# Kernel tuning notes

Hardware: AMD Instinct MI355X
Metric: run time of the kernel (lower is better)

## Reference

```python
import jax, jax.numpy as jnp
import numpy as np

SIZE = 256

def _linear(x, W, b):
    # torch nn.Linear: y = x @ W^T + b, W has shape [out, in]
    return jnp.einsum('bsd,ed->bse', x, W) + b

def setup_inputs() -> dict:
    key = jax.random.key(0)
    ks = jax.random.split(key, 10)
    B, Sq, Sk, D = 8, 2048, 2048, SIZE
    s = 1.0 / np.sqrt(D)
    return {
        'x': jax.random.normal(ks[0], (B, Sq, D), jnp.float32),
        'states': jax.random.normal(ks[1], (B, Sk, D), jnp.float32),
        'Wq': jax.random.normal(ks[2], (D, D), jnp.float32) * s,
        'bq': jnp.zeros((D,), jnp.float32),
        'Wk': jax.random.normal(ks[3], (D, D), jnp.float32) * s,
        'bk': jnp.zeros((D,), jnp.float32),
        'Wv': jax.random.normal(ks[4], (D, D), jnp.float32) * s,
        'bv': jnp.zeros((D,), jnp.float32),
        'Wa': jax.random.normal(ks[5], (D, D), jnp.float32) * s,  # LuongAttention.fc
        'ba': jnp.zeros((D,), jnp.float32),
    }

def reference(x, states, Wq, bq, Wk, bk, Wv, bv, Wa, ba):
    q = _linear(x, Wq, bq)          # [B,Sq,D]
    k = _linear(states, Wk, bk)     # [B,Sk,D]
    v = _linear(states, Wv, bv)     # [B,Sk,D]
    wk = _linear(k, Wa, ba)         # [B,Sk,D]
    scores = jnp.einsum('bqd,bkd->bqk', q, wk)   # bmm(q, wk^T)
    scores = jax.nn.softmax(scores, axis=-1)
    # original: (v[:,None,:,:] * scores[...,None]).sum(-2) == matmul
    context = jnp.einsum('bqk,bkd->bqd', scores, v)
    return context
```

## Files before the change

kernel.cpp:

```cpp
#include <hip/hip_runtime.h>
#include <cstdint>
#include <cstddef>

typedef _Float16 half_t;
typedef _Float16 half8 __attribute__((ext_vector_type(8)));
typedef _Float16 half4v __attribute__((ext_vector_type(4)));
typedef float float4_ __attribute__((ext_vector_type(4)));

#define NB 8
#define SEQ 2048
#define DIM 256
#define NROWS (NB*SEQ)
#define KS 4
#define NIT 16

__device__ __forceinline__ void dma16(const half_t* g, half_t* l) {
    __builtin_amdgcn_global_load_lds(
        (const __attribute__((address_space(1))) void*)g,
        (__attribute__((address_space(3))) void*)l,
        16, 0, 0);
}

__global__ __launch_bounds__(256) void prep_kernel(
    const float* __restrict__ Wq, const float* __restrict__ Wk,
    const float* __restrict__ Wv, const float* __restrict__ Wa,
    const float* __restrict__ bq,
    half_t* __restrict__ M_hi, half_t* __restrict__ M_lo,
    half_t* __restrict__ Wk_hi, half_t* __restrict__ Wk_lo,
    half_t* __restrict__ Wv_hi, float* __restrict__ bq2)
{
    const int d = blockIdx.x;
    const int m = threadIdx.x;
    const int idx = d * 256 + m;
    float acc = 0.f;
    for (int e = 0; e < 256; ++e)
        acc += Wa[e * 256 + d] * Wq[e * 256 + m];
    half_t h = (half_t)acc;
    M_hi[idx] = h;
    M_lo[idx] = (half_t)(acc - (float)h);
    float wk = Wk[idx];
    h = (half_t)wk;
    Wk_hi[idx] = h;
    Wk_lo[idx] = (half_t)(wk - (float)h);
    Wv_hi[idx] = (half_t)Wv[idx];
    if (m == 0) {
        float b2 = 0.f;
        for (int e = 0; e < 256; ++e) b2 += bq[e] * Wa[e * 256 + d];
        bq2[d] = b2;
    }
}

__global__ __launch_bounds__(256, 2) void linear_kernel(
    const float* __restrict__ x, const float* __restrict__ states,
    const half_t* __restrict__ M_hi, const half_t* __restrict__ M_lo, const float* __restrict__ bq2,
    const half_t* __restrict__ Wk_hi, const half_t* __restrict__ Wk_lo, const float* __restrict__ bk,
    const half_t* __restrict__ Wv_hi, const float* __restrict__ bv,
    half_t* __restrict__ q2_hi,
    half_t* __restrict__ k_hi,
    half_t* __restrict__ vT)
{
    __shared__ half_t sB[2 * 64 * 256];
    half_t* sBh = sB;
    half_t* sBl = sB + 64 * 256;

    const int seg  = blockIdx.x >> 8;
    const int t    = blockIdx.x & 255;
    const int tid  = threadIdx.x;
    const int lane = tid & 63;
    const int wv   = tid >> 6;
    const int quad = lane >> 4;
    const int l15  = lane & 15;
    const int rb   = t * 64;
    const int r0   = rb + wv * 16;

    const float* src  = (seg == 0) ? x : states;
    const half_t* Bh  = (seg == 0) ? M_hi : (seg == 1) ? Wk_hi : Wv_hi;
    const half_t* Bl  = (seg == 0) ? M_lo : Wk_lo;
    const float* bias = (seg == 0) ? bq2 : (seg == 1) ? bk : bv;

    half8 ah[8], al[8];
    #pragma unroll
    for (int c = 0; c < 8; ++c) {
        const float* pa = src + (size_t)(r0 + l15) * 256 + c * 32 + quad * 8;
        float4_ u0 = *(const float4_*)pa;
        float4_ u1 = *(const float4_*)(pa + 4);
        #pragma unroll
        for (int j = 0; j < 4; ++j) {
            half_t hh = (half_t)u0[j];
            ah[c][j] = hh; al[c][j] = (half_t)(u0[j] - (float)hh);
            hh = (half_t)u1[j];
            ah[c][4 + j] = hh; al[c][4 + j] = (half_t)(u1[j] - (float)hh);
        }
    }

    float4_ acc[16];
    if (seg != 2) {
        #pragma unroll
        for (int nt = 0; nt < 16; ++nt) {
            float be = bias[nt * 16 + l15];
            acc[nt] = {be, be, be, be};
        }
    } else {
        #pragma unroll
        for (int et = 0; et < 16; ++et)
            #pragma unroll
            for (int r = 0; r < 4; ++r)
                acc[et][r] = bias[et * 16 + quad * 4 + r];
    }

    #pragma unroll
    for (int eg = 0; eg < 4; ++eg) {
        __syncthreads();
        #pragma unroll
        for (int i = 0; i < 8; ++i) {
            int g = tid + i * 256;
            int e = g >> 5, c = g & 31;
            *(half8*)(sBh + e * 256 + ((c ^ (e & 7)) * 8)) =
                *(const half8*)(Bh + (size_t)(eg * 64 + e) * 256 + c * 8);
        }
        if (seg != 2) {
            #pragma unroll
            for (int i = 0; i < 8; ++i) {
                int g = tid + i * 256;
                int e = g >> 5, c = g & 31;
                *(half8*)(sBl + e * 256 + ((c ^ (e & 7)) * 8)) =
                    *(const half8*)(Bl + (size_t)(eg * 64 + e) * 256 + c * 8);
            }
        }
        __syncthreads();

        if (seg != 2) {
            #pragma unroll
            for (int ntl = 0; ntl < 4; ++ntl) {
                float4_ a = acc[eg * 4 + ntl];
                const int el = ntl * 16 + l15;
                #pragma unroll
                for (int c = 0; c < 8; ++c) {
                    int off = el * 256 + (((c * 4 + quad) ^ (el & 7)) * 8);
                    half8 bh = *(const half8*)(sBh + off);
                    half8 bl = *(const half8*)(sBl + off);
                    a = __builtin_amdgcn_mfma_f32_16x16x32_f16(ah[c], bh, a, 0, 0, 0);
                    a = __builtin_amdgcn_mfma_f32_16x16x32_f16(al[c], bh, a, 0, 0, 0);
                    a = __builtin_amdgcn_mfma_f32_16x16x32_f16(ah[c], bl, a, 0, 0, 0);
                }
                acc[eg * 4 + ntl] = a;
            }
        } else {
            #pragma unroll
            for (int ntl = 0; ntl < 4; ++ntl) {
                float4_ a = acc[eg * 4 + ntl];
                const int el = ntl * 16 + l15;
                #pragma unroll
                for (int c = 0; c < 8; ++c) {
                    int off = el * 256 + (((c * 4 + quad) ^ (el & 7)) * 8);
                    half8 aw = *(const half8*)(sBh + off);
                    a = __builtin_amdgcn_mfma_f32_16x16x32_f16(aw, ah[c], a, 0, 0, 0);
                }
                acc[eg * 4 + ntl] = a;
            }
        }
    }

    __syncthreads();
    if (seg != 2) {
        half_t* R = sB;
        #pragma unroll
        for (int nt = 0; nt < 16; ++nt)
            #pragma unroll
            for (int r = 0; r < 4; ++r)
                R[(wv * 16 + quad * 4 + r) * 256 + nt * 16 + l15] = (half_t)acc[nt][r];
        __syncthreads();
        if (seg == 0) {
            for (int i = 0; i < 8; ++i) {
                int g = tid + i * 256;
                int row = g >> 5, cc = g & 31;
                *(half8*)(q2_hi + (size_t)(rb + row) * 256 + cc * 8) =
                    *(const half8*)(R + row * 256 + cc * 8);
            }
        } else {
            for (int i = 0; i < 8; ++i) {
                int g = tid + i * 256;
                int row = g >> 5, cc = g & 31;
                int s = row & 31;
                size_t dst = ((size_t)(rb + row) >> 5) * 8192 + s * 256 + ((cc ^ (s & 7)) * 8);
                *(half8*)(k_hi + dst) = *(const half8*)(R + row * 256 + cc * 8);
            }
        }
    } else {
        half_t* sV = sB;
        #pragma unroll
        for (int et = 0; et < 16; ++et)
            #pragma unroll
            for (int r = 0; r < 4; ++r)
                sV[(et * 16 + quad * 4 + r) * 68 + wv * 16 + l15] = (half_t)acc[et][r];
        __syncthreads();
        const int b = rb >> 11, s0 = rb & 2047;
        for (int i = 0; i < 8; ++i) {
            int g = tid + i * 256;
            int d = g >> 3, sc8 = g & 7;
            int kt = (s0 >> 5) + (sc8 >> 2);
            int q  = sc8 & 3;
            int t32 = (sc8 >> 2) * 32;
            int slot = q ^ (d & 3) ^ ((d >> 2) & 3);
            half4v a4 = *(const half4v*)(sV + d * 68 + t32 + q * 4);
            half4v b4 = *(const half4v*)(sV + d * 68 + t32 + 16 + q * 4);
            half8 hv;
            hv[0] = a4[0]; hv[1] = a4[1]; hv[2] = a4[2]; hv[3] = a4[3];
            hv[4] = b4[0]; hv[5] = b4[1]; hv[6] = b4[2]; hv[7] = b4[3];
            size_t dst = ((size_t)b * 64 + kt) * 8192 + d * 32 + slot * 8;
            *(half8*)(vT + dst) = hv;
        }
    }
}

__global__ __launch_bounds__(256, 2) void attn_kernel(
    const half_t* __restrict__ q2_hi,
    const half_t* __restrict__ k_hi, const half_t* __restrict__ vT,
    half_t* __restrict__ pc, float* __restrict__ pm, float* __restrict__ pl)
{
    __shared__ __align__(16) unsigned char smem[64 * 1024];
    float* scr = (float*)smem;

    const int tid  = threadIdx.x;
    const int lane = tid & 63;
    const int wv   = tid >> 6;
    const int quad = lane >> 4;
    const int l15  = lane & 15;

    const int b  = blockIdx.x & 7;
    const int qt = (blockIdx.x >> 3) & 15;
    const int ks = blockIdx.x >> 7;

    const int qbase = b * 2048 + qt * 128 + wv * 32;

    half8 qf[2][8];
    #pragma unroll
    for (int ct = 0; ct < 2; ++ct)
        #pragma unroll
        for (int c = 0; c < 8; ++c)
            qf[ct][c] = *(const half8*)(q2_hi +
                (size_t)(qbase + ct * 16 + l15) * 256 + c * 32 + quad * 8);

    float4_ ctx[16][2];
    #pragma unroll
    for (int dt = 0; dt < 16; ++dt) {
        ctx[dt][0] = {0.f, 0.f, 0.f, 0.f};
        ctx[dt][1] = {0.f, 0.f, 0.f, 0.f};
    }
    float m_c[2] = {-1e30f, -1e30f};
    float l_c[2] = {0.f, 0.f};

    const half_t* kh_b = k_hi + (size_t)b * 64 * 8192;
    const half_t* vt_b = vT   + (size_t)b * 64 * 8192;
    const int t0 = ks * NIT;

    const int vslot8 = (quad ^ (l15 & 3) ^ ((l15 >> 2) & 3)) * 8;

    {
        const half_t* kt_ = kh_b + (size_t)t0 * 8192;
        #pragma unroll
        for (int i = 0; i < 4; ++i) {
            const int sg = i * 4 + wv;
            dma16(kt_ + sg * 512 + lane * 8, (half_t*)smem + sg * 512);
        }
        const half_t* vt_ = vt_b + (size_t)t0 * 8192;
        #pragma unroll
        for (int i = 0; i < 4; ++i) {
            const int sg = i * 4 + wv;
            dma16(vt_ + sg * 512 + lane * 8, (half_t*)(smem + 32768) + sg * 512);
        }
    }

    half8 pfp[2];
    #pragma unroll
    for (int ct = 0; ct < 2; ++ct)
        #pragma unroll
        for (int j = 0; j < 8; ++j) pfp[ct][j] = (half_t)0;

    for (int it = 0; it < NIT; ++it) {
        half_t* s_k  = (half_t*)(smem + ((it & 1) << 14));
        half_t* s_vP = (half_t*)(smem + 32768 + (((it + 1) & 1) << 14));
        const bool pre = (it + 1 < NIT);

        asm volatile("s_waitcnt vmcnt(4)" ::: "memory");
        __builtin_amdgcn_s_barrier();
        asm volatile("" ::: "memory");

        if (pre) {
            const half_t* kt_ = kh_b + (size_t)(t0 + it + 1) * 8192;
            half_t* kdst = (half_t*)(smem + (((it + 1) & 1) << 14));
            #pragma unroll
            for (int i = 0; i < 4; ++i) {
                const int sg = i * 4 + wv;
                dma16(kt_ + sg * 512 + lane * 8, kdst + sg * 512);
            }
        }

        float4_ S[2][2];
        S[0][0] = {0.f,0.f,0.f,0.f}; S[0][1] = {0.f,0.f,0.f,0.f};
        S[1][0] = {0.f,0.f,0.f,0.f}; S[1][1] = {0.f,0.f,0.f,0.f};
        __builtin_amdgcn_s_setprio(1);
        #pragma unroll
        for (int c = 0; c < 8; ++c)
            #pragma unroll
            for (int kt = 0; kt < 2; ++kt) {
                const int key = kt * 16 + l15;
                const int off = key * 256 + (((c * 4 + quad) ^ (key & 7)) * 8);
                half8 kf = *(const half8*)(s_k + off);
                #pragma unroll
                for (int ct = 0; ct < 2; ++ct)
                    S[kt][ct] = __builtin_amdgcn_mfma_f32_16x16x32_f16(kf, qf[ct][c], S[kt][ct], 0, 0, 0);
            }
        __builtin_amdgcn_s_setprio(0);

        float mx0, mx1;
        {
            float a0 = fmaxf(fmaxf(S[0][0][0], S[0][0][1]), fmaxf(S[0][0][2], S[0][0][3]));
            float b0 = fmaxf(fmaxf(S[1][0][0], S[1][0][1]), fmaxf(S[1][0][2], S[1][0][3]));
            mx0 = fmaxf(a0, b0);
            mx0 = fmaxf(mx0, __shfl_xor(mx0, 16));
            mx0 = fmaxf(mx0, __shfl_xor(mx0, 32));
            float a1 = fmaxf(fmaxf(S[0][1][0], S[0][1][1]), fmaxf(S[0][1][2], S[0][1][3]));
            float b1 = fmaxf(fmaxf(S[1][1][0], S[1][1][1]), fmaxf(S[1][1][2], S[1][1][3]));
            mx1 = fmaxf(a1, b1);
            mx1 = fmaxf(mx1, __shfl_xor(mx1, 16));
            mx1 = fmaxf(mx1, __shfl_xor(mx1, 32));
        }
        const int doresc = __any((mx0 > m_c[0] + 8.f) || (mx1 > m_c[1] + 8.f));
        float alpha0 = 1.f, alpha1 = 1.f;
        if (doresc) {
            float mn0 = fmaxf(m_c[0], mx0);
            float mn1 = fmaxf(m_c[1], mx1);
            alpha0 = __expf(m_c[0] - mn0);
            alpha1 = __expf(m_c[1] - mn1);
            m_c[0] = mn0; m_c[1] = mn1;
        }

        __builtin_amdgcn_s_setprio(1);
        if (it > 0) {
            #pragma unroll
            for (int dt = 0; dt < 16; ++dt) {
                half8 vf = *(const half8*)(s_vP + (dt * 16 + l15) * 32 + vslot8);
                ctx[dt][0] = __builtin_amdgcn_mfma_f32_16x16x32_f16(vf, pfp[0], ctx[dt][0], 0, 0, 0);
                ctx[dt][1] = __builtin_amdgcn_mfma_f32_16x16x32_f16(vf, pfp[1], ctx[dt][1], 0, 0, 0);
            }
        }

        half8 pfc[2];
        #pragma unroll
        for (int ct = 0; ct < 2; ++ct) {
            const float mm = m_c[ct];
            float rs = 0.f;
            #pragma unroll
            for (int r = 0; r < 4; ++r) {
                float p0 = __expf(S[0][ct][r] - mm);
                float p1 = __expf(S[1][ct][r] - mm);
                rs += p0 + p1;
                pfc[ct][r]     = (half_t)p0;
                pfc[ct][4 + r] = (half_t)p1;
            }
            rs += __shfl_xor(rs, 16);
            rs += __shfl_xor(rs, 32);
            l_c[ct] = l_c[ct] * (ct ? alpha1 : alpha0) + rs;
        }
        __builtin_amdgcn_s_setprio(0);

        if (doresc) {
            #pragma unroll
            for (int dt = 0; dt < 16; ++dt)
                #pragma unroll
                for (int r = 0; r < 4; ++r) {
                    ctx[dt][0][r] *= alpha0;
                    ctx[dt][1][r] *= alpha1;
                }
        }

        pfp[0] = pfc[0];
        pfp[1] = pfc[1];

        if (pre) {
            __builtin_amdgcn_sched_barrier(0);
            __builtin_amdgcn_s_barrier();
            asm volatile("" ::: "memory");
            const half_t* vt_ = vt_b + (size_t)(t0 + it + 1) * 8192;
            half_t* vdst = (half_t*)(smem + 32768 + (((it + 1) & 1) << 14));
            #pragma unroll
            for (int i = 0; i < 4; ++i) {
                const int sg = i * 4 + wv;
                dma16(vt_ + sg * 512 + lane * 8, vdst + sg * 512);
            }
        }
    }

    asm volatile("s_waitcnt vmcnt(0)" ::: "memory");
    __builtin_amdgcn_s_barrier();
    asm volatile("" ::: "memory");
    {
        half_t* s_v = (half_t*)(smem + 32768 + (((NIT - 1) & 1) << 14));
        __builtin_amdgcn_s_setprio(1);
        #pragma unroll
        for (int dt = 0; dt < 16; ++dt) {
            half8 vf = *(const half8*)(s_v + (dt * 16 + l15) * 32 + vslot8);
            ctx[dt][0] = __builtin_amdgcn_mfma_f32_16x16x32_f16(vf, pfp[0], ctx[dt][0], 0, 0, 0);
            ctx[dt][1] = __builtin_amdgcn_mfma_f32_16x16x32_f16(vf, pfp[1], ctx[dt][1], 0, 0, 0);
        }
        __builtin_amdgcn_s_setprio(0);
    }

    float rinv[2] = {1.0f / l_c[0], 1.0f / l_c[1]};
    float* sw = scr + wv * (32 * 68);
    half_t* pcs = pc + (size_t)ks * NROWS * 256;
    #pragma unroll
    for (int rd = 0; rd < 4; ++rd) {
        #pragma unroll
        for (int dtl = 0; dtl < 4; ++dtl) {
            const int dt = rd * 4 + dtl;
            #pragma unroll
            for (int ct = 0; ct < 2; ++ct)
                #pragma unroll
                for (int r = 0; r < 4; ++r)
                    sw[(ct * 16 + l15) * 68 + dtl * 16 + quad * 4 + r] = ctx[dt][ct][r] * rinv[ct];
        }
        #pragma unroll
        for (int i = 0; i < 8; ++i) {
            int g = lane + i * 64;
            int q = g >> 4, dc = g & 15;
            float4_ v4 = *(const float4_*)(sw + q * 68 + dc * 4);
            half4v h4;
            #pragma unroll
            for (int j = 0; j < 4; ++j) h4[j] = (half_t)v4[j];
            *(half4v*)(pcs + (size_t)(qbase + q) * 256 + rd * 64 + dc * 4) = h4;
        }
    }
    if (quad == 0) {
        #pragma unroll
        for (int ct = 0; ct < 2; ++ct) {
            const size_t row = qbase + ct * 16 + l15;
            pm[(size_t)ks * NROWS + row] = m_c[ct];
            pl[(size_t)ks * NROWS + row] = l_c[ct];
        }
    }
}

__global__ __launch_bounds__(256) void combine_kernel(
    const half_t* __restrict__ pc, const float* __restrict__ pm,
    const float* __restrict__ pl, float* __restrict__ out)
{
    const int t = threadIdx.x;
    const int row = blockIdx.x * 4 + (t >> 6);
    const int d0 = (t & 63) * 4;
    float m[KS], l[KS];
    float ms = -1e30f;
    #pragma unroll
    for (int i = 0; i < KS; ++i) {
        m[i] = pm[(size_t)i * NROWS + row];
        l[i] = pl[(size_t)i * NROWS + row];
        ms = fmaxf(ms, m[i]);
    }
    float w[KS], tot = 0.f;
    #pragma unroll
    for (int i = 0; i < KS; ++i) {
        w[i] = l[i] * __expf(m[i] - ms);
        tot += w[i];
    }
    float inv = 1.0f / tot;
    float4_ o = {0.f, 0.f, 0.f, 0.f};
    #pragma unroll
    for (int i = 0; i < KS; ++i) {
        half4v y = *(const half4v*)(pc + ((size_t)i * NROWS + row) * 256 + d0);
        float wi = w[i] * inv;
        #pragma unroll
        for (int j = 0; j < 4; ++j) o[j] += wi * (float)y[j];
    }
    *(float4_*)(out + (size_t)row * 256 + d0) = o;
}

extern "C" void kernel_launch(void* const* d_in, const int* in_sizes, int n_in,
                              void* d_out, int out_size, void* d_ws, size_t ws_size,
                              hipStream_t stream) {
    const float* x      = (const float*)d_in[0];
    const float* states = (const float*)d_in[1];
    const float* Wq     = (const float*)d_in[2];
    const float* bq     = (const float*)d_in[3];
    const float* Wk     = (const float*)d_in[4];
    const float* bk     = (const float*)d_in[5];
    const float* Wv     = (const float*)d_in[6];
    const float* bv     = (const float*)d_in[7];
    const float* Wa     = (const float*)d_in[8];
    float* out = (float*)d_out;

    char* ws = (char*)d_ws;
    size_t off = 0;
    auto alloc = [&](size_t bytes) -> void* {
        void* p = ws + off;
        off += (bytes + 255) & ~(size_t)255;
        return p;
    };
    half_t* M_hi  = (half_t*)alloc(65536 * 2);
    half_t* M_lo  = (half_t*)alloc(65536 * 2);
    half_t* Wk_hi = (half_t*)alloc(65536 * 2);
    half_t* Wk_lo = (half_t*)alloc(65536 * 2);
    half_t* Wv_hi = (half_t*)alloc(65536 * 2);
    float*  bq2   = (float*)alloc(256 * 4);
    half_t* q2_hi = (half_t*)alloc((size_t)NROWS * 256 * 2);
    half_t* k_hi  = (half_t*)alloc((size_t)NROWS * 256 * 2);
    half_t* vT    = (half_t*)alloc((size_t)NROWS * 256 * 2);
    half_t* pc    = (half_t*)alloc((size_t)KS * NROWS * 256 * 2);
    float*  pm    = (float*)alloc((size_t)KS * NROWS * 4);
    float*  pl    = (float*)alloc((size_t)KS * NROWS * 4);

    prep_kernel<<<256, 256, 0, stream>>>(Wq, Wk, Wv, Wa, bq,
                                         M_hi, M_lo, Wk_hi, Wk_lo, Wv_hi, bq2);
    linear_kernel<<<768, 256, 0, stream>>>(x, states,
                                           M_hi, M_lo, bq2,
                                           Wk_hi, Wk_lo, bk,
                                           Wv_hi, bv,
                                           q2_hi, k_hi, vT);
    attn_kernel<<<8 * 16 * KS, 256, 0, stream>>>(q2_hi, k_hi, vT,
                                                 pc, pm, pl);
    combine_kernel<<<NROWS / 4, 256, 0, stream>>>(pc, pm, pl, out);
}
```

Before: 196.8 us.

## Interleave PV MFMAs with QK MFMAs and defer cross-lane softmax reductions

Moves the previous tile's P·V MFMAs into the QK score loop so the two matrix streams interleave, and issues the V prefetch earlier, right after the score loop. Per-lane row sums are now kept unreduced and shuffled only once at the end. The max reduction across lanes now runs only when a rescale is triggered. This removes shuffle latency from the inner loop and gives the scheduler more independent MFMA work, at the cost of higher register pressure and a changed barrier placement. Lanes can now see different partial maxima before reduction, and correctness rests on the lazy-rescale threshold.

```diff
diff --git a/kernel.cpp b/kernel.cpp
--- a/kernel.cpp
+++ b/kernel.cpp
@@ -301,7 +301,7 @@
         S[1][0] = {0.f,0.f,0.f,0.f}; S[1][1] = {0.f,0.f,0.f,0.f};
         __builtin_amdgcn_s_setprio(1);
         #pragma unroll
-        for (int c = 0; c < 8; ++c)
+        for (int c = 0; c < 8; ++c) {
             #pragma unroll
             for (int kt = 0; kt < 2; ++kt) {
                 const int key = kt * 16 + l15;
@@ -311,41 +311,53 @@
                 for (int ct = 0; ct < 2; ++ct)
                     S[kt][ct] = __builtin_amdgcn_mfma_f32_16x16x32_f16(kf, qf[ct][c], S[kt][ct], 0, 0, 0);
             }
+            if (it > 0) {
+                #pragma unroll
+                for (int dl = 0; dl < 2; ++dl) {
+                    const int dt = c * 2 + dl;
+                    half8 vf = *(const half8*)(s_vP + (dt * 16 + l15) * 32 + vslot8);
+                    ctx[dt][0] = __builtin_amdgcn_mfma_f32_16x16x32_f16(vf, pfp[0], ctx[dt][0], 0, 0, 0);
+                    ctx[dt][1] = __builtin_amdgcn_mfma_f32_16x16x32_f16(vf, pfp[1], ctx[dt][1], 0, 0, 0);
+                }
+            }
+        }
         __builtin_amdgcn_s_setprio(0);
+        __builtin_amdgcn_sched_barrier(0);
+        __builtin_amdgcn_s_barrier();
+        asm volatile("" ::: "memory");
+
+        if (pre) {
+            const half_t* vt_ = vt_b + (size_t)(t0 + it + 1) * 8192;
+            half_t* vdst = (half_t*)(smem + 32768 + (((it + 1) & 1) << 14));
+            #pragma unroll
+            for (int i = 0; i < 4; ++i) {
+                const int sg = i * 4 + wv;
+                dma16(vt_ + sg * 512 + lane * 8, vdst + sg * 512);
+            }
+        }
 
         float mx0, mx1;
         {
             float a0 = fmaxf(fmaxf(S[0][0][0], S[0][0][1]), fmaxf(S[0][0][2], S[0][0][3]));
             float b0 = fmaxf(fmaxf(S[1][0][0], S[1][0][1]), fmaxf(S[1][0][2], S[1][0][3]));
             mx0 = fmaxf(a0, b0);
-            mx0 = fmaxf(mx0, __shfl_xor(mx0, 16));
-            mx0 = fmaxf(mx0, __shfl_xor(mx0, 32));
             float a1 = fmaxf(fmaxf(S[0][1][0], S[0][1][1]), fmaxf(S[0][1][2], S[0][1][3]));
             float b1 = fmaxf(fmaxf(S[1][1][0], S[1][1][1]), fmaxf(S[1][1][2], S[1][1][3]));
             mx1 = fmaxf(a1, b1);
-            mx1 = fmaxf(mx1, __shfl_xor(mx1, 16));
-            mx1 = fmaxf(mx1, __shfl_xor(mx1, 32));
         }
         const int doresc = __any((mx0 > m_c[0] + 8.f) || (mx1 > m_c[1] + 8.f));
         float alpha0 = 1.f, alpha1 = 1.f;
         if (doresc) {
-            float mn0 = fmaxf(m_c[0], mx0);
-            float mn1 = fmaxf(m_c[1], mx1);
+            float r0 = fmaxf(mx0, __shfl_xor(mx0, 16));
+            r0 = fmaxf(r0, __shfl_xor(r0, 32));
+            float r1 = fmaxf(mx1, __shfl_xor(mx1, 16));
+            r1 = fmaxf(r1, __shfl_xor(r1, 32));
+            float mn0 = fmaxf(m_c[0], r0);
+            float mn1 = fmaxf(m_c[1], r1);
             alpha0 = __expf(m_c[0] - mn0);
             alpha1 = __expf(m_c[1] - mn1);
             m_c[0] = mn0; m_c[1] = mn1;
         }
-
-        __builtin_amdgcn_s_setprio(1);
-        if (it > 0) {
-            #pragma unroll
-            for (int dt = 0; dt < 16; ++dt) {
-                half8 vf = *(const half8*)(s_vP + (dt * 16 + l15) * 32 + vslot8);
-                ctx[dt][0] = __builtin_amdgcn_mfma_f32_16x16x32_f16(vf, pfp[0], ctx[dt][0], 0, 0, 0);
-                ctx[dt][1] = __builtin_amdgcn_mfma_f32_16x16x32_f16(vf, pfp[1], ctx[dt][1], 0, 0, 0);
-            }
-        }
-
         half8 pfc[2];
         #pragma unroll
         for (int ct = 0; ct < 2; ++ct) {
@@ -359,12 +371,8 @@
                 pfc[ct][r]     = (half_t)p0;
                 pfc[ct][4 + r] = (half_t)p1;
             }
-            rs += __shfl_xor(rs, 16);
-            rs += __shfl_xor(rs, 32);
             l_c[ct] = l_c[ct] * (ct ? alpha1 : alpha0) + rs;
         }
-        __builtin_amdgcn_s_setprio(0);
-
         if (doresc) {
             #pragma unroll
             for (int dt = 0; dt < 16; ++dt)
@@ -374,22 +382,8 @@
                     ctx[dt][1][r] *= alpha1;
                 }
         }
-
         pfp[0] = pfc[0];
         pfp[1] = pfc[1];
-
-        if (pre) {
-            __builtin_amdgcn_sched_barrier(0);
-            __builtin_amdgcn_s_barrier();
-            asm volatile("" ::: "memory");
-            const half_t* vt_ = vt_b + (size_t)(t0 + it + 1) * 8192;
-            half_t* vdst = (half_t*)(smem + 32768 + (((it + 1) & 1) << 14));
-            #pragma unroll
-            for (int i = 0; i < 4; ++i) {
-                const int sg = i * 4 + wv;
-                dma16(vt_ + sg * 512 + lane * 8, vdst + sg * 512);
-            }
-        }
     }
 
     asm volatile("s_waitcnt vmcnt(0)" ::: "memory");
@@ -407,7 +401,16 @@
         __builtin_amdgcn_s_setprio(0);
     }
 
-    float rinv[2] = {1.0f / l_c[0], 1.0f / l_c[1]};
+    float lt[2];
+    #pragma unroll
+    for (int ct = 0; ct < 2; ++ct) {
+        float s = l_c[ct];
+        s += __shfl_xor(s, 16);
+        s += __shfl_xor(s, 32);
+        lt[ct] = s;
+    }
+
+    float rinv[2] = {1.0f / lt[0], 1.0f / lt[1]};
     float* sw = scr + wv * (32 * 68);
     half_t* pcs = pc + (size_t)ks * NROWS * 256;
     #pragma unroll
@@ -437,7 +440,7 @@
         for (int ct = 0; ct < 2; ++ct) {
             const size_t row = qbase + ct * 16 + l15;
             pm[(size_t)ks * NROWS + row] = m_c[ct];
-            pl[(size_t)ks * NROWS + row] = l_c[ct];
+            pl[(size_t)ks * NROWS + row] = lt[ct];
         }
     }
 }
```

After: 198.3 us. No clear change (+0.8%).
